# Kernel tuning notes

Hardware: AMD Instinct MI355X
Metric: run time of the kernel (lower is better)

## Reference

```python
import jax, jax.numpy as jnp
import numpy as np

BITS = 32  # container = uint32 -> 32 bits per word


def _pack_sign_bits(x):
    """Faithful jax port of np.signbit -> np.packbits -> .view(uint32).

    np.packbits is MSB-first within each byte; .view(uint32) then
    reinterprets groups of 4 bytes little-endian. We reproduce both.
    """
    n = x.shape[0]
    pad = (-n) % BITS  # zero-pad to a multiple of 32 (numpy.resize fills 0)
    if pad:
        x = jnp.concatenate([x, jnp.zeros((pad,), dtype=x.dtype)])
    bits = jnp.signbit(x).astype(jnp.uint32).reshape(-1, 4, 8)  # [words, byte, bit]
    bit_w = jnp.left_shift(jnp.uint32(1), (7 - jnp.arange(8)).astype(jnp.uint32))   # MSB-first in byte
    byte_w = jnp.left_shift(jnp.uint32(1), (8 * jnp.arange(4)).astype(jnp.uint32))  # little-endian bytes
    weights = byte_w[:, None] * bit_w[None, :]  # [4, 8] uint32
    return jnp.sum(bits * weights[None, :, :], axis=(1, 2), dtype=jnp.uint32)  # [n/32] uint32


def setup_inputs() -> dict:
    key = jax.random.key(0)
    N = 134217728  # 2^27 floats, multiple of 32
    x = jax.random.normal(key, (N,), dtype=jnp.float32)
    return {"x": x}


def reference(x):
    return _pack_sign_bits(x)
```

## Files before the change

kernel.cpp:

```cpp
#include <hip/hip_runtime.h>
#include <stdint.h>


__global__ __launch_bounds__(256) void PackBits_61289183314094_kernel(
    const uint4* __restrict__ x4, uint32_t* __restrict__ out, int nwords) {
  int w = blockIdx.x * blockDim.x + threadIdx.x;
  if (w >= nwords) return;

  const uint4* p = x4 + (size_t)w * 8;

  uint32_t nat = 0;
#pragma unroll
  for (int k = 0; k < 8; ++k) {
    uint4 v = p[k];
    nat |= (v.x >> 31) << (4 * k + 0);
    nat |= (v.y >> 31) << (4 * k + 1);
    nat |= (v.z >> 31) << (4 * k + 2);
    nat |= (v.w >> 31) << (4 * k + 3);
  }

  out[w] = __builtin_bswap32(__brev(nat));
}

extern "C" void kernel_launch(void* const* d_in, const int* in_sizes, int n_in,
                              void* d_out, int out_size, void* d_ws, size_t ws_size,
                              hipStream_t stream) {
  const uint4* x4 = (const uint4*)d_in[0];
  uint32_t* out = (uint32_t*)d_out;
  int n = in_sizes[0];
  int nwords = n / 32;

  const int threads = 256;
  int blocks = (nwords + threads - 1) / threads;
  PackBits_61289183314094_kernel<<<blocks, threads, 0, stream>>>(x4, out, nwords);
}
```

Baseline: 675.1 us.

## Coalesce loads: one uint4 per thread, combine nibbles via warp shuffles

Each thread now loads a single contiguous uint4 instead of eight strided uint4s per output word. Adjacent threads therefore read adjacent 16-byte chunks, so global loads are fully coalesced. Groups of 8 lanes OR their sign nibbles together with xor-shuffles, and one lane per group writes the packed word. The cost is 8x more threads, three shuffles per thread, and output stores made by only one lane in eight.

```diff
diff --git a/kernel.cpp b/kernel.cpp
--- a/kernel.cpp
+++ b/kernel.cpp
@@ -3,23 +3,23 @@
 
 
 __global__ __launch_bounds__(256) void PackBits_61289183314094_kernel(
-    const uint4* __restrict__ x4, uint32_t* __restrict__ out, int nwords) {
-  int w = blockIdx.x * blockDim.x + threadIdx.x;
-  if (w >= nwords) return;
+    const uint4* __restrict__ x4, uint32_t* __restrict__ out, int n4) {
+  int gid = blockIdx.x * blockDim.x + threadIdx.x;
+  if (gid >= n4) return;
 
-  const uint4* p = x4 + (size_t)w * 8;
+  uint4 v = x4[gid];
 
-  uint32_t nat = 0;
-#pragma unroll
-  for (int k = 0; k < 8; ++k) {
-    uint4 v = p[k];
-    nat |= (v.x >> 31) << (4 * k + 0);
-    nat |= (v.y >> 31) << (4 * k + 1);
-    nat |= (v.z >> 31) << (4 * k + 2);
-    nat |= (v.w >> 31) << (4 * k + 3);
+  int lane = threadIdx.x & 63;
+  uint32_t nib = (v.x >> 31) | ((v.y >> 31) << 1) | ((v.z >> 31) << 2) |
+                 ((v.w >> 31) << 3);
+  uint32_t part = nib << (4 * (lane & 7));
+  part |= __shfl_xor(part, 1);
+  part |= __shfl_xor(part, 2);
+  part |= __shfl_xor(part, 4);
+
+  if ((lane & 7) == 0) {
+    out[gid >> 3] = __builtin_bswap32(__brev(part));
   }
-
-  out[w] = __builtin_bswap32(__brev(nat));
 }
 
 extern "C" void kernel_launch(void* const* d_in, const int* in_sizes, int n_in,
@@ -28,9 +28,9 @@
   const uint4* x4 = (const uint4*)d_in[0];
   uint32_t* out = (uint32_t*)d_out;
   int n = in_sizes[0];
-  int nwords = n / 32;
+  int n4 = n / 4;
 
   const int threads = 256;
-  int blocks = (nwords + threads - 1) / threads;
-  PackBits_61289183314094_kernel<<<blocks, threads, 0, stream>>>(x4, out, nwords);
+  int blocks = (n4 + threads - 1) / threads;
+  PackBits_61289183314094_kernel<<<blocks, threads, 0, stream>>>(x4, out, n4);
 }
```

New measurement: 652.1 us. -3.4%, faster.
